# Performance work log

Measured on AMD Instinct MI355X. Metric: run time of the kernel, lower is better.

## Reference

```python
import jax, jax.numpy as jnp
import numpy as np

T, B, D, H, NQ = 512, 128, 512, 64, 64  # seq_len, batch, input_dim, hidden_dim == n_qubits
EPS = 1e-5

def setup_inputs() -> dict:
    key = jax.random.key(0)
    ks = jax.random.split(key, 11)
    s = 0.05
    return {
        "inputs": jax.random.normal(ks[0], (T, B, D), jnp.float32),
        "W0": jax.random.normal(ks[1], (4, NQ, D + H), jnp.float32) * s,
        "b0": jax.random.normal(ks[2], (4, NQ), jnp.float32) * s,
        "th0": jax.random.normal(ks[3], (4, NQ), jnp.float32) * s,
        "g0": jnp.ones((H,), jnp.float32),
        "be0": jnp.zeros((H,), jnp.float32),
        "W1": jax.random.normal(ks[4], (4, NQ, H + H), jnp.float32) * s,
        "b1": jax.random.normal(ks[5], (4, NQ), jnp.float32) * s,
        "th1": jax.random.normal(ks[6], (4, NQ), jnp.float32) * s,
        "g1": jnp.ones((H,), jnp.float32),
        "be1": jnp.zeros((H,), jnp.float32),
    }

def _qlstm_layer(x, W, b, th, gamma, beta):
    # x: [T, B, Din]. Faithful to source: h_prev = c_prev = 0 at EVERY timestep
    # (the torch code never writes back `states` inside the time loop), so all
    # timesteps are independent and fully vectorized.
    zeros_h = jnp.zeros(x.shape[:-1] + (H,), x.dtype)
    combined = jnp.concatenate([x, zeros_h], axis=-1)           # [T,B,Din+H]
    # 4 gate linears stacked on leading axis g: forget, input, update, output
    z = jnp.einsum('tbk,gnk->gtbn', combined, W) + b[:, None, None, :]
    # quantum circuit closed form: RX(z_i+th_i) per qubit + CNOT ladder + <Z_k>
    #   => cumprod_{i<=k} cos(z_i + th_i)
    q = jnp.cumprod(jnp.cos(z + th[:, None, None, :]), axis=-1)  # [4,T,B,NQ]
    sg = jax.nn.sigmoid(q)
    i_g = sg[1]
    g_g = jnp.tanh(sg[2])
    o_g = sg[3]
    # c = f * c_prev + i * g, with c_prev == 0  (f gate has no effect)
    c = i_g * g_g                                                # [T,B,H]
    h = o_g * jnp.tanh(c)
    mu = jnp.mean(h, axis=-1, keepdims=True)
    var = jnp.mean((h - mu) ** 2, axis=-1, keepdims=True)
    h_ln = (h - mu) * jax.lax.rsqrt(var + EPS) * gamma + beta
    return h_ln, c

def reference(inputs, W0, b0, th0, g0, be0, W1, b1, th1, g1, be1):
    h0, c0 = _qlstm_layer(inputs, W0, b0, th0, g0, be0)  # layer 0 (no dropout: p=0)
    h1, c1 = _qlstm_layer(h0, W1, b1, th1, g1, be1)      # layer 1
    outputs = h1                                          # [T,B,H]
    # new_states = states at the last timestep: [(h_ln, c)] per layer
    return (outputs, h0[-1], c0[-1], h1[-1], c1[-1])
```

## Files before the change

### kernel.cpp

```cpp
#include <hip/hip_runtime.h>
#include <hip/hip_bf16.h>

typedef __attribute__((ext_vector_type(8))) short bf16x8;
typedef __attribute__((ext_vector_type(4))) float f32x4;

#define T_SEQ   512
#define B_BATCH 128
#define H_DIM   64
#define MB      64
#define A1S     72
#define ZS_STRIDE 193
#define A2S       72
#define LASTROW ((T_SEQ - 1) * B_BATCH)

#define W0H 0
#define W0M 98304
#define W0L 196608
#define W1H 294912
#define W1M 307200
#define W1L 319488

__device__ __forceinline__ void tsplit(float f, unsigned& h, unsigned& m, unsigned& l) {
    unsigned uf = __builtin_bit_cast(unsigned, f);
    h = uf >> 16;
    float hf = __builtin_bit_cast(float, uf & 0xFFFF0000u);
    float r1 = f - hf;
    unsigned u1 = __builtin_bit_cast(unsigned, r1);
    m = u1 >> 16;
    float mf = __builtin_bit_cast(float, u1 & 0xFFFF0000u);
    float r2 = r1 - mf;
    l = __builtin_bit_cast(unsigned, r2) >> 16;
}

__device__ __forceinline__ void tsplit2(float a, float b,
                                        unsigned& ph, unsigned& pm, unsigned& pl) {
    unsigned ha, ma, la, hb, mb, lb;
    tsplit(a, ha, ma, la);
    tsplit(b, hb, mb, lb);
    ph = ha | (hb << 16);
    pm = ma | (mb << 16);
    pl = la | (lb << 16);
}

__device__ __forceinline__ void split16(const float4 f[4],
                                        short* __restrict__ ah, short* __restrict__ am,
                                        short* __restrict__ al, int ao) {
    uint4 Ph, Pm, Pl;
    tsplit2(f[0].x, f[0].y, Ph.x, Pm.x, Pl.x);
    tsplit2(f[0].z, f[0].w, Ph.y, Pm.y, Pl.y);
    tsplit2(f[1].x, f[1].y, Ph.z, Pm.z, Pl.z);
    tsplit2(f[1].z, f[1].w, Ph.w, Pm.w, Pl.w);
    *(uint4*)(ah + ao) = Ph;
    *(uint4*)(am + ao) = Pm;
    *(uint4*)(al + ao) = Pl;
    tsplit2(f[2].x, f[2].y, Ph.x, Pm.x, Pl.x);
    tsplit2(f[2].z, f[2].w, Ph.y, Pm.y, Pl.y);
    tsplit2(f[3].x, f[3].y, Ph.z, Pm.z, Pl.z);
    tsplit2(f[3].z, f[3].w, Ph.w, Pm.w, Pl.w);
    *(uint4*)(ah + ao + 8) = Ph;
    *(uint4*)(am + ao + 8) = Pm;
    *(uint4*)(al + ao + 8) = Pl;
}

__device__ __forceinline__ f32x4 mfma6(bf16x8 ah, bf16x8 am, bf16x8 al,
                                       bf16x8 bh, bf16x8 bm, bf16x8 bl, f32x4 c) {
    c = __builtin_amdgcn_mfma_f32_16x16x32_bf16(ah, bh, c, 0, 0, 0);
    c = __builtin_amdgcn_mfma_f32_16x16x32_bf16(ah, bm, c, 0, 0, 0);
    c = __builtin_amdgcn_mfma_f32_16x16x32_bf16(am, bh, c, 0, 0, 0);
    c = __builtin_amdgcn_mfma_f32_16x16x32_bf16(ah, bl, c, 0, 0, 0);
    c = __builtin_amdgcn_mfma_f32_16x16x32_bf16(al, bh, c, 0, 0, 0);
    c = __builtin_amdgcn_mfma_f32_16x16x32_bf16(am, bm, c, 0, 0, 0);
    return c;
}

__device__ __forceinline__ float fast_cos(float x) {
    float n = rintf(x * 0.6366197723675814f);
    int   m = (int)n;
    float r = __builtin_fmaf(n, -1.5707962512969971e+00f, x);
    r = __builtin_fmaf(n, -7.5497894158615964e-08f, r);
    r = __builtin_fmaf(n, -5.3903025299577647e-15f, r);
    float r2 = r * r;
    float ps = __builtin_fmaf(r2, 2.7557314297e-06f, -1.9841270114e-04f);
    ps = __builtin_fmaf(r2, ps, 8.3333337680e-03f);
    ps = __builtin_fmaf(r2, ps, -1.6666667163e-01f);
    float s = __builtin_fmaf(r * r2, ps, r);
    float pc = __builtin_fmaf(r2, 2.4801587642e-05f, -1.3888889225e-03f);
    pc = __builtin_fmaf(r2, pc, 4.1666667908e-02f);
    pc = __builtin_fmaf(r2, pc, -0.5f);
    float c = __builtin_fmaf(r2, pc, 1.0f);
    float v = (m & 1) ? s : c;
    unsigned sign = (unsigned)((m + 1) & 2) << 30;
    return __builtin_bit_cast(float, __builtin_bit_cast(unsigned, v) ^ sign);
}

__device__ __forceinline__ float fast_sigmoid(float x) {
    float e = __expf(-x);
    float d = 1.0f + e;
    float r = __builtin_amdgcn_rcpf(d);
    return r * (2.0f - d * r);
}

__device__ __forceinline__ float fast_tanh_pos(float x) {
    float t = __expf(2.0f * x);
    float d = t + 1.0f;
    float r = __builtin_amdgcn_rcpf(d);
    r = r * (2.0f - d * r);
    return (t - 1.0f) * r;
}

__global__ __launch_bounds__(256) void presplit_w(const float* __restrict__ W0,
                                                  const float* __restrict__ W1,
                                                  short* __restrict__ ws) {
    int i = blockIdx.x * 256 + threadIdx.x;
    if (i < 98304) {
        int r = i >> 9, k = i & 511;
        unsigned h, m, l;
        tsplit(W0[(r + 64) * 576 + k], h, m, l);
        ws[W0H + i] = (short)h;
        ws[W0M + i] = (short)m;
        ws[W0L + i] = (short)l;
    } else if (i < 110592) {
        int j = i - 98304;
        int r = j >> 6, k = j & 63;
        unsigned h, m, l;
        tsplit(W1[(r + 64) * 128 + k], h, m, l);
        ws[W1H + j] = (short)h;
        ws[W1M + j] = (short)m;
        ws[W1L + j] = (short)l;
    }
}

__global__ __launch_bounds__(256, 3) void qlstm_fused(
    const float* __restrict__ x,
    const float* __restrict__ b0,
    const float* __restrict__ th0,
    const float* __restrict__ g0,
    const float* __restrict__ be0,
    const float* __restrict__ b1,
    const float* __restrict__ th1,
    const float* __restrict__ g1,
    const float* __restrict__ be1,
    const short* __restrict__ wsp,
    float* __restrict__ out)
{
    __shared__ __align__(16) char lds[50944];
    short* ah = (short*)lds;
    short* am = ah + 64 * A1S;
    short* al = am + 64 * A1S;
    float* zs  = (float*)lds;
    short* a2h = (short*)lds;
    short* a2m = a2h + 64 * A2S;
    short* a2l = a2m + 64 * A2S;
    float* bt0 = (float*)(lds + 49408);
    float* bt1 = bt0 + 192;

    const int tid = threadIdx.x;
    const long rowbase = (long)blockIdx.x * MB;

    float* out0 = out;
    float* out1 = out + (long)T_SEQ * B_BATCH * H_DIM;
    float* out2 = out1 + B_BATCH * H_DIM;
    float* out3 = out2 + B_BATCH * H_DIM;
    float* out4 = out3 + B_BATCH * H_DIM;

    if (tid < 192) {
        bt0[tid] = b0[64 + tid] + th0[64 + tid];
        bt1[tid] = b1[64 + tid] + th1[64 + tid];
    }

    const int lane = tid & 63;
    const int wave = tid >> 6;
    const int ln   = lane & 15;
    const int quad = lane >> 4;
    const int cw   = wave * 48;

    int brow0[3], brow1[3];
    for (int nt = 0; nt < 3; ++nt) {
        int gc = cw + nt * 16 + ln;
        brow0[nt] = gc * 512;
        brow1[nt] = gc * 64;
    }

    const int sr = tid >> 2;
    const int sc = (tid & 3) << 4;
    const float* xrow = x + (rowbase + sr) * 512 + sc;
    const int sao = sr * A1S + sc;

    f32x4 acc[4][3];
    #pragma unroll
    for (int mt = 0; mt < 4; ++mt)
        #pragma unroll
        for (int nt = 0; nt < 3; ++nt)
            acc[mt][nt] = (f32x4){0.f, 0.f, 0.f, 0.f};

    {
        float4 f[4];
        #pragma unroll
        for (int u = 0; u < 4; ++u) f[u] = *(const float4*)(xrow + u * 4);
        split16(f, ah, am, al, sao);
    }
    __syncthreads();

    for (int kc = 0; kc < 512; kc += 64) {
        float4 nf[4];
        const bool more = (kc + 64) < 512;
        if (more) {
            #pragma unroll
            for (int u = 0; u < 4; ++u)
                nf[u] = *(const float4*)(xrow + kc + 64 + u * 4);
        }
        #pragma unroll
        for (int k0 = 0; k0 < 64; k0 += 32) {
            int ka = k0 + quad * 8;
            bf16x8 Ah[4], Am[4], Al[4];
            #pragma unroll
            for (int mt = 0; mt < 4; ++mt) {
                int ao = (mt * 16 + ln) * A1S + ka;
                Ah[mt] = *(const bf16x8*)(ah + ao);
                Am[mt] = *(const bf16x8*)(am + ao);
                Al[mt] = *(const bf16x8*)(al + ao);
            }
            #pragma unroll
            for (int nt = 0; nt < 3; ++nt) {
                int bo = brow0[nt] + kc + ka;
                bf16x8 Bh = *(const bf16x8*)(wsp + W0H + bo);
                bf16x8 Bm = *(const bf16x8*)(wsp + W0M + bo);
                bf16x8 Bl = *(const bf16x8*)(wsp + W0L + bo);
                #pragma unroll
                for (int mt = 0; mt < 4; ++mt)
                    acc[mt][nt] = mfma6(Ah[mt], Am[mt], Al[mt], Bh, Bm, Bl, acc[mt][nt]);
            }
        }
        __syncthreads();
        if (more) {
            split16(nf, ah, am, al, sao);
            __syncthreads();
        }
    }

    #pragma unroll
    for (int mt = 0; mt < 4; ++mt)
        #pragma unroll
        for (int nt = 0; nt < 3; ++nt)
            #pragma unroll
            for (int i = 0; i < 4; ++i) {
                int row = mt * 16 + quad * 4 + i;
                int col = cw + nt * 16 + ln;
                zs[row * ZS_STRIDE + col] = acc[mt][nt][i];
            }
    __syncthreads();

    if (tid < 192) {
        int gi = tid >> 6;
        int r  = tid & 63;
        float* zrow = zs + r * ZS_STRIDE + gi * 64;
        const float* btg = bt0 + gi * 64;
        float p = 1.0f;
        for (int n = 0; n < 64; ++n) {
            p *= fast_cos(zrow[n] + btg[n]);
            zrow[n] = p;
        }
    }
    __syncthreads();

    {
        int r = tid >> 2;
        int j = tid & 3;
        long tbrow = rowbase + r;
        bool lastt = (tbrow >= LASTROW);
        int bidx = (int)(tbrow - LASTROW);
        const float* zr = zs + r * ZS_STRIDE;
        float h[16];
        float s = 0.f;
        #pragma unroll
        for (int i = 0; i < 16; ++i) {
            int n = j * 16 + i;
            float q1 = zr[n];
            float q2 = zr[64 + n];
            float q3 = zr[128 + n];
            float ig = fast_sigmoid(q1);
            float gg = fast_tanh_pos(fast_sigmoid(q2));
            float og = fast_sigmoid(q3);
            float c  = ig * gg;
            float hv = og * fast_tanh_pos(c);
            h[i] = hv;
            s += hv;
            if (lastt) out2[bidx * 64 + n] = c;
        }
        s += __shfl_xor(s, 1);  s += __shfl_xor(s, 2);
        float mu = s * (1.0f / 64.0f);
        float s2 = 0.f;
        #pragma unroll
        for (int i = 0; i < 16; ++i) {
            float d = h[i] - mu;
            s2 += d * d;
        }
        s2 += __shfl_xor(s2, 1); s2 += __shfl_xor(s2, 2);
        float var = s2 * (1.0f / 64.0f);
        float rs  = rsqrtf(var + 1e-5f);
        float hl[16];
        #pragma unroll
        for (int i = 0; i < 16; ++i) {
            int n = j * 16 + i;
            hl[i] = (h[i] - mu) * rs * g0[n] + be0[n];
            if (lastt) out1[bidx * 64 + n] = hl[i];
        }
        __syncthreads();

        int ab = r * A2S + j * 16;
        uint4 Ph, Pm, Pl;
        tsplit2(hl[0], hl[1], Ph.x, Pm.x, Pl.x);
        tsplit2(hl[2], hl[3], Ph.y, Pm.y, Pl.y);
        tsplit2(hl[4], hl[5], Ph.z, Pm.z, Pl.z);
        tsplit2(hl[6], hl[7], Ph.w, Pm.w, Pl.w);
        *(uint4*)(a2h + ab) = Ph;
        *(uint4*)(a2m + ab) = Pm;
        *(uint4*)(a2l + ab) = Pl;
        tsplit2(hl[8],  hl[9],  Ph.x, Pm.x, Pl.x);
        tsplit2(hl[10], hl[11], Ph.y, Pm.y, Pl.y);
        tsplit2(hl[12], hl[13], Ph.z, Pm.z, Pl.z);
        tsplit2(hl[14], hl[15], Ph.w, Pm.w, Pl.w);
        *(uint4*)(a2h + ab + 8) = Ph;
        *(uint4*)(a2m + ab + 8) = Pm;
        *(uint4*)(a2l + ab + 8) = Pl;
    }
    __syncthreads();

    f32x4 acc2[4][3];
    #pragma unroll
    for (int mt = 0; mt < 4; ++mt)
        #pragma unroll
        for (int nt = 0; nt < 3; ++nt)
            acc2[mt][nt] = (f32x4){0.f, 0.f, 0.f, 0.f};
    #pragma unroll
    for (int k0 = 0; k0 < 64; k0 += 32) {
        int ka = k0 + quad * 8;
        bf16x8 Ah[4], Am[4], Al[4];
        #pragma unroll
        for (int mt = 0; mt < 4; ++mt) {
            int ao = (mt * 16 + ln) * A2S + ka;
            Ah[mt] = *(const bf16x8*)(a2h + ao);
            Am[mt] = *(const bf16x8*)(a2m + ao);
            Al[mt] = *(const bf16x8*)(a2l + ao);
        }
        #pragma unroll
        for (int nt = 0; nt < 3; ++nt) {
            int bo = brow1[nt] + ka;
            bf16x8 Bh = *(const bf16x8*)(wsp + W1H + bo);
            bf16x8 Bm = *(const bf16x8*)(wsp + W1M + bo);
            bf16x8 Bl = *(const bf16x8*)(wsp + W1L + bo);
            #pragma unroll
            for (int mt = 0; mt < 4; ++mt)
                acc2[mt][nt] = mfma6(Ah[mt], Am[mt], Al[mt], Bh, Bm, Bl, acc2[mt][nt]);
        }
    }
    __syncthreads();
    #pragma unroll
    for (int mt = 0; mt < 4; ++mt)
        #pragma unroll
        for (int nt = 0; nt < 3; ++nt)
            #pragma unroll
            for (int i = 0; i < 4; ++i) {
                int row = mt * 16 + quad * 4 + i;
                int col = cw + nt * 16 + ln;
                zs[row * ZS_STRIDE + col] = acc2[mt][nt][i];
            }
    __syncthreads();

    if (tid < 192) {
        int gi = tid >> 6;
        int r  = tid & 63;
        float* zrow = zs + r * ZS_STRIDE + gi * 64;
        const float* btg = bt1 + gi * 64;
        float p = 1.0f;
        for (int n = 0; n < 64; ++n) {
            p *= fast_cos(zrow[n] + btg[n]);
            zrow[n] = p;
        }
    }
    __syncthreads();

    {
        int r = tid >> 2;
        int j = tid & 3;
        long tbrow = rowbase + r;
        bool lastt = (tbrow >= LASTROW);
        int bidx = (int)(tbrow - LASTROW);
        const float* zr = zs + r * ZS_STRIDE;
        float h[16];
        float s = 0.f;
        #pragma unroll
        for (int i = 0; i < 16; ++i) {
            int n = j * 16 + i;
            float q1 = zr[n];
            float q2 = zr[64 + n];
            float q3 = zr[128 + n];
            float ig = fast_sigmoid(q1);
            float gg = fast_tanh_pos(fast_sigmoid(q2));
            float og = fast_sigmoid(q3);
            float c  = ig * gg;
            float hv = og * fast_tanh_pos(c);
            h[i] = hv;
            s += hv;
            if (lastt) out4[bidx * 64 + n] = c;
        }
        s += __shfl_xor(s, 1);  s += __shfl_xor(s, 2);
        float mu = s * (1.0f / 64.0f);
        float s2 = 0.f;
        #pragma unroll
        for (int i = 0; i < 16; ++i) {
            float d = h[i] - mu;
            s2 += d * d;
        }
        s2 += __shfl_xor(s2, 1); s2 += __shfl_xor(s2, 2);
        float var = s2 * (1.0f / 64.0f);
        float rs  = rsqrtf(var + 1e-5f);
        float o4[16];
        #pragma unroll
        for (int i = 0; i < 16; ++i)
            o4[i] = (h[i] - mu) * rs * g1[j * 16 + i] + be1[j * 16 + i];
        float* dst = out0 + tbrow * 64 + j * 16;
        #pragma unroll
        for (int i4 = 0; i4 < 4; ++i4)
            *(float4*)(dst + i4 * 4) = *(float4*)(o4 + i4 * 4);
        if (lastt) {
            float* dst3 = out3 + (long)bidx * 64 + j * 16;
            #pragma unroll
            for (int i4 = 0; i4 < 4; ++i4)
                *(float4*)(dst3 + i4 * 4) = *(float4*)(o4 + i4 * 4);
        }
    }
}

extern "C" void kernel_launch(void* const* d_in, const int* in_sizes, int n_in,
                              void* d_out, int out_size, void* d_ws, size_t ws_size,
                              hipStream_t stream) {
    const float* x   = (const float*)d_in[0];
    const float* W0  = (const float*)d_in[1];
    const float* b0  = (const float*)d_in[2];
    const float* th0 = (const float*)d_in[3];
    const float* g0  = (const float*)d_in[4];
    const float* be0 = (const float*)d_in[5];
    const float* W1  = (const float*)d_in[6];
    const float* b1  = (const float*)d_in[7];
    const float* th1 = (const float*)d_in[8];
    const float* g1  = (const float*)d_in[9];
    const float* be1 = (const float*)d_in[10];
    short* wsp = (short*)d_ws;

    presplit_w<<<dim3(432), dim3(256), 0, stream>>>(W0, W1, wsp);
    qlstm_fused<<<dim3(1024), dim3(256), 0, stream>>>(
        x, b0, th0, g0, be0, b1, th1, g1, be1, wsp, (float*)d_out);
}
```

Before: 321.9 us.

## Process gate epilogue in 16-row quarters to shrink LDS and raise occupancy

The z staging buffer now holds only 16 rows at a time. The cumprod and LayerNorm epilogues loop over four quarters, and the layer-2 A operand gets its own LDS region. This cuts LDS from about 50KB to 40KB, and launch bounds rise from 3 to 4 blocks per CU. The cost is much less parallelism in the epilogue: only 48 or 64 threads are active per quarter, with many more __syncthreads. Bias plus theta is now read from global memory inside the loop instead of being precomputed in LDS.

New measurement: 408.8 us. 27.0% more time.

```diff
diff --git a/kernel.cpp b/kernel.cpp
--- a/kernel.cpp
+++ b/kernel.cpp
@@ -9,7 +9,7 @@
 #define H_DIM   64
 #define MB      64
 #define A1S     72
-#define ZS_STRIDE 193
+#define ZQ_STRIDE 193
 #define A2S       72
 #define LASTROW ((T_SEQ - 1) * B_BATCH)
 
@@ -130,7 +130,7 @@
     }
 }
 
-__global__ __launch_bounds__(256, 3) void qlstm_fused(
+__global__ __launch_bounds__(256, 4) void qlstm_fused(
     const float* __restrict__ x,
     const float* __restrict__ b0,
     const float* __restrict__ th0,
@@ -143,16 +143,14 @@
     const short* __restrict__ wsp,
     float* __restrict__ out)
 {
-    __shared__ __align__(16) char lds[50944];
+    __shared__ __align__(16) char lds[40000];
     short* ah = (short*)lds;
     short* am = ah + 64 * A1S;
     short* al = am + 64 * A1S;
     float* zs  = (float*)lds;
-    short* a2h = (short*)lds;
+    short* a2h = (short*)(lds + 12352);
     short* a2m = a2h + 64 * A2S;
     short* a2l = a2m + 64 * A2S;
-    float* bt0 = (float*)(lds + 49408);
-    float* bt1 = bt0 + 192;
 
     const int tid = threadIdx.x;
     const long rowbase = (long)blockIdx.x * MB;
@@ -162,11 +160,6 @@
     float* out2 = out1 + B_BATCH * H_DIM;
     float* out3 = out2 + B_BATCH * H_DIM;
     float* out4 = out3 + B_BATCH * H_DIM;
-
-    if (tid < 192) {
-        bt0[tid] = b0[64 + tid] + th0[64 + tid];
-        bt1[tid] = b1[64 + tid] + th1[64 + tid];
-    }
 
     const int lane = tid & 63;
     const int wave = tid >> 6;
@@ -239,90 +232,89 @@
     }
 
     #pragma unroll
-    for (int mt = 0; mt < 4; ++mt)
+    for (int qd = 0; qd < 4; ++qd) {
+        if (qd > 0) __syncthreads();
         #pragma unroll
         for (int nt = 0; nt < 3; ++nt)
             #pragma unroll
-            for (int i = 0; i < 4; ++i) {
-                int row = mt * 16 + quad * 4 + i;
-                int col = cw + nt * 16 + ln;
-                zs[row * ZS_STRIDE + col] = acc[mt][nt][i];
-            }
-    __syncthreads();
-
-    if (tid < 192) {
-        int gi = tid >> 6;
-        int r  = tid & 63;
-        float* zrow = zs + r * ZS_STRIDE + gi * 64;
-        const float* btg = bt0 + gi * 64;
-        float p = 1.0f;
-        for (int n = 0; n < 64; ++n) {
-            p *= fast_cos(zrow[n] + btg[n]);
-            zrow[n] = p;
-        }
-    }
-    __syncthreads();
-
-    {
-        int r = tid >> 2;
-        int j = tid & 3;
-        long tbrow = rowbase + r;
-        bool lastt = (tbrow >= LASTROW);
-        int bidx = (int)(tbrow - LASTROW);
-        const float* zr = zs + r * ZS_STRIDE;
-        float h[16];
-        float s = 0.f;
-        #pragma unroll
-        for (int i = 0; i < 16; ++i) {
-            int n = j * 16 + i;
-            float q1 = zr[n];
-            float q2 = zr[64 + n];
-            float q3 = zr[128 + n];
-            float ig = fast_sigmoid(q1);
-            float gg = fast_tanh_pos(fast_sigmoid(q2));
-            float og = fast_sigmoid(q3);
-            float c  = ig * gg;
-            float hv = og * fast_tanh_pos(c);
-            h[i] = hv;
-            s += hv;
-            if (lastt) out2[bidx * 64 + n] = c;
-        }
-        s += __shfl_xor(s, 1);  s += __shfl_xor(s, 2);
-        float mu = s * (1.0f / 64.0f);
-        float s2 = 0.f;
-        #pragma unroll
-        for (int i = 0; i < 16; ++i) {
-            float d = h[i] - mu;
-            s2 += d * d;
-        }
-        s2 += __shfl_xor(s2, 1); s2 += __shfl_xor(s2, 2);
-        float var = s2 * (1.0f / 64.0f);
-        float rs  = rsqrtf(var + 1e-5f);
-        float hl[16];
-        #pragma unroll
-        for (int i = 0; i < 16; ++i) {
-            int n = j * 16 + i;
-            hl[i] = (h[i] - mu) * rs * g0[n] + be0[n];
-            if (lastt) out1[bidx * 64 + n] = hl[i];
-        }
-        __syncthreads();
-
-        int ab = r * A2S + j * 16;
-        uint4 Ph, Pm, Pl;
-        tsplit2(hl[0], hl[1], Ph.x, Pm.x, Pl.x);
-        tsplit2(hl[2], hl[3], Ph.y, Pm.y, Pl.y);
-        tsplit2(hl[4], hl[5], Ph.z, Pm.z, Pl.z);
-        tsplit2(hl[6], hl[7], Ph.w, Pm.w, Pl.w);
-        *(uint4*)(a2h + ab) = Ph;
-        *(uint4*)(a2m + ab) = Pm;
-        *(uint4*)(a2l + ab) = Pl;
-        tsplit2(hl[8],  hl[9],  Ph.x, Pm.x, Pl.x);
-        tsplit2(hl[10], hl[11], Ph.y, Pm.y, Pl.y);
-        tsplit2(hl[12], hl[13], Ph.z, Pm.z, Pl.z);
-        tsplit2(hl[14], hl[15], Ph.w, Pm.w, Pl.w);
-        *(uint4*)(a2h + ab + 8) = Ph;
-        *(uint4*)(a2m + ab + 8) = Pm;
-        *(uint4*)(a2l + ab + 8) = Pl;
+            for (int i = 0; i < 4; ++i)
+                zs[(quad * 4 + i) * ZQ_STRIDE + cw + nt * 16 + ln] = acc[qd][nt][i];
+        __syncthreads();
+
+        if (tid < 48) {
+            int gi = tid >> 4;
+            int r  = tid & 15;
+            float* zrow = zs + r * ZQ_STRIDE + gi * 64;
+            const float* bg = b0 + 64 + gi * 64;
+            const float* tg = th0 + 64 + gi * 64;
+            float p = 1.0f;
+            for (int n = 0; n < 64; ++n) {
+                p *= fast_cos(zrow[n] + bg[n] + tg[n]);
+                zrow[n] = p;
+            }
+        }
+        __syncthreads();
+
+        if (tid < 64) {
+            int r = tid >> 2;
+            int j = tid & 3;
+            int rloc = qd * 16 + r;
+            long tbrow = rowbase + rloc;
+            bool lastt = (tbrow >= LASTROW);
+            int bidx = (int)(tbrow - LASTROW);
+            const float* zr = zs + r * ZQ_STRIDE;
+            float h[16];
+            float s = 0.f;
+            #pragma unroll
+            for (int i = 0; i < 16; ++i) {
+                int n = j * 16 + i;
+                float q1 = zr[n];
+                float q2 = zr[64 + n];
+                float q3 = zr[128 + n];
+                float ig = fast_sigmoid(q1);
+                float gg = fast_tanh_pos(fast_sigmoid(q2));
+                float og = fast_sigmoid(q3);
+                float c  = ig * gg;
+                float hv = og * fast_tanh_pos(c);
+                h[i] = hv;
+                s += hv;
+                if (lastt) out2[bidx * 64 + n] = c;
+            }
+            s += __shfl_xor(s, 1);  s += __shfl_xor(s, 2);
+            float mu = s * (1.0f / 64.0f);
+            float s2 = 0.f;
+            #pragma unroll
+            for (int i = 0; i < 16; ++i) {
+                float d = h[i] - mu;
+                s2 += d * d;
+            }
+            s2 += __shfl_xor(s2, 1); s2 += __shfl_xor(s2, 2);
+            float var = s2 * (1.0f / 64.0f);
+            float rs  = rsqrtf(var + 1e-5f);
+            float hl[16];
+            #pragma unroll
+            for (int i = 0; i < 16; ++i) {
+                int n = j * 16 + i;
+                hl[i] = (h[i] - mu) * rs * g0[n] + be0[n];
+                if (lastt) out1[bidx * 64 + n] = hl[i];
+            }
+            int ab = rloc * A2S + j * 16;
+            uint4 Ph, Pm, Pl;
+            tsplit2(hl[0], hl[1], Ph.x, Pm.x, Pl.x);
+            tsplit2(hl[2], hl[3], Ph.y, Pm.y, Pl.y);
+            tsplit2(hl[4], hl[5], Ph.z, Pm.z, Pl.z);
+            tsplit2(hl[6], hl[7], Ph.w, Pm.w, Pl.w);
+            *(uint4*)(a2h + ab) = Ph;
+            *(uint4*)(a2m + ab) = Pm;
+            *(uint4*)(a2l + ab) = Pl;
+            tsplit2(hl[8],  hl[9],  Ph.x, Pm.x, Pl.x);
+            tsplit2(hl[10], hl[11], Ph.y, Pm.y, Pl.y);
+            tsplit2(hl[12], hl[13], Ph.z, Pm.z, Pl.z);
+            tsplit2(hl[14], hl[15], Ph.w, Pm.w, Pl.w);
+            *(uint4*)(a2h + ab + 8) = Ph;
+            *(uint4*)(a2m + ab + 8) = Pm;
+            *(uint4*)(a2l + ab + 8) = Pl;
+        }
     }
     __syncthreads();
 
@@ -354,80 +346,80 @@
                 acc2[mt][nt] = mfma6(Ah[mt], Am[mt], Al[mt], Bh, Bm, Bl, acc2[mt][nt]);
         }
     }
-    __syncthreads();
+
     #pragma unroll
-    for (int mt = 0; mt < 4; ++mt)
+    for (int qd = 0; qd < 4; ++qd) {
+        __syncthreads();
         #pragma unroll
         for (int nt = 0; nt < 3; ++nt)
             #pragma unroll
-            for (int i = 0; i < 4; ++i) {
-                int row = mt * 16 + quad * 4 + i;
-                int col = cw + nt * 16 + ln;
-                zs[row * ZS_STRIDE + col] = acc2[mt][nt][i];
-            }
-    __syncthreads();
-
-    if (tid < 192) {
-        int gi = tid >> 6;
-        int r  = tid & 63;
-        float* zrow = zs + r * ZS_STRIDE + gi * 64;
-        const float* btg = bt1 + gi * 64;
-        float p = 1.0f;
-        for (int n = 0; n < 64; ++n) {
-            p *= fast_cos(zrow[n] + btg[n]);
-            zrow[n] = p;
-        }
-    }
-    __syncthreads();
-
-    {
-        int r = tid >> 2;
-        int j = tid & 3;
-        long tbrow = rowbase + r;
-        bool lastt = (tbrow >= LASTROW);
-        int bidx = (int)(tbrow - LASTROW);
-        const float* zr = zs + r * ZS_STRIDE;
-        float h[16];
-        float s = 0.f;
-        #pragma unroll
-        for (int i = 0; i < 16; ++i) {
-            int n = j * 16 + i;
-            float q1 = zr[n];
-            float q2 = zr[64 + n];
-            float q3 = zr[128 + n];
-            float ig = fast_sigmoid(q1);
-            float gg = fast_tanh_pos(fast_sigmoid(q2));
-            float og = fast_sigmoid(q3);
-            float c  = ig * gg;
-            float hv = og * fast_tanh_pos(c);
-            h[i] = hv;
-            s += hv;
-            if (lastt) out4[bidx * 64 + n] = c;
-        }
-        s += __shfl_xor(s, 1);  s += __shfl_xor(s, 2);
-        float mu = s * (1.0f / 64.0f);
-        float s2 = 0.f;
-        #pragma unroll
-        for (int i = 0; i < 16; ++i) {
-            float d = h[i] - mu;
-            s2 += d * d;
-        }
-        s2 += __shfl_xor(s2, 1); s2 += __shfl_xor(s2, 2);
-        float var = s2 * (1.0f / 64.0f);
-        float rs  = rsqrtf(var + 1e-5f);
-        float o4[16];
-        #pragma unroll
-        for (int i = 0; i < 16; ++i)
-            o4[i] = (h[i] - mu) * rs * g1[j * 16 + i] + be1[j * 16 + i];
-        float* dst = out0 + tbrow * 64 + j * 16;
-        #pragma unroll
-        for (int i4 = 0; i4 < 4; ++i4)
-            *(float4*)(dst + i4 * 4) = *(float4*)(o4 + i4 * 4);
-        if (lastt) {
-            float* dst3 = out3 + (long)bidx * 64 + j * 16;
+            for (int i = 0; i < 4; ++i)
+                zs[(quad * 4 + i) * ZQ_STRIDE + cw + nt * 16 + ln] = acc2[qd][nt][i];
+        __syncthreads();
+
+        if (tid < 48) {
+            int gi = tid >> 4;
+            int r  = tid & 15;
+            float* zrow = zs + r * ZQ_STRIDE + gi * 64;
+            const float* bg = b1 + 64 + gi * 64;
+            const float* tg = th1 + 64 + gi * 64;
+            float p = 1.0f;
+            for (int n = 0; n < 64; ++n) {
+                p *= fast_cos(zrow[n] + bg[n] + tg[n]);
+                zrow[n] = p;
+            }
+        }
+        __syncthreads();
+
+        if (tid < 64) {
+            int r = tid >> 2;
+            int j = tid & 3;
+            long tbrow = rowbase + qd * 16 + r;
+            bool lastt = (tbrow >= LASTROW);
+            int bidx = (int)(tbrow - LASTROW);
+            const float* zr = zs + r * ZQ_STRIDE;
+            float h[16];
+            float s = 0.f;
+            #pragma unroll
+            for (int i = 0; i < 16; ++i) {
+                int n = j * 16 + i;
+                float q1 = zr[n];
+                float q2 = zr[64 + n];
+                float q3 = zr[128 + n];
+                float ig = fast_sigmoid(q1);
+                float gg = fast_tanh_pos(fast_sigmoid(q2));
+                float og = fast_sigmoid(q3);
+                float c  = ig * gg;
+                float hv = og * fast_tanh_pos(c);
+                h[i] = hv;
+                s += hv;
+                if (lastt) out4[bidx * 64 + n] = c;
+            }
+            s += __shfl_xor(s, 1);  s += __shfl_xor(s, 2);
+            float mu = s * (1.0f / 64.0f);
+            float s2 = 0.f;
+            #pragma unroll
+            for (int i = 0; i < 16; ++i) {
+                float d = h[i] - mu;
+                s2 += d * d;
+            }
+            s2 += __shfl_xor(s2, 1); s2 += __shfl_xor(s2, 2);
+            float var = s2 * (1.0f / 64.0f);
+            float rs  = rsqrtf(var + 1e-5f);
+            float o4[16];
+            #pragma unroll
+            for (int i = 0; i < 16; ++i)
+                o4[i] = (h[i] - mu) * rs * g1[j * 16 + i] + be1[j * 16 + i];
+            float* dst = out0 + tbrow * 64 + j * 16;
             #pragma unroll
             for (int i4 = 0; i4 < 4; ++i4)
-                *(float4*)(dst3 + i4 * 4) = *(float4*)(o4 + i4 * 4);
+                *(float4*)(dst + i4 * 4) = *(float4*)(o4 + i4 * 4);
+            if (lastt) {
+                float* dst3 = out3 + (long)bidx * 64 + j * 16;
+                #pragma unroll
+                for (int i4 = 0; i4 < 4; ++i4)
+                    *(float4*)(dst3 + i4 * 4) = *(float4*)(o4 + i4 * 4);
+            }
         }
     }
 }
```

## Double-buffer layer-0 A tiles in LDS and drop redundant barriers

Applied to the files above, without the earlier changes.

Splits the layer-0 activation staging into two LDS buffers so the next K-chunk is written while the current one is read, cutting one barrier per iteration. The layer-1 activation buffer moves to its own LDS region so it no longer aliases zs, which lets two more barriers go. LDS grows to about 77 KB and launch bounds drop from 3 to 2 blocks per CU, trading occupancy for fewer syncs.

Result: faster. 314.1 us (-2.4%).

```diff
diff --git a/kernel.cpp b/kernel.cpp
--- a/kernel.cpp
+++ b/kernel.cpp
@@ -130,7 +130,7 @@
     }
 }
 
-__global__ __launch_bounds__(256, 3) void qlstm_fused(
+__global__ __launch_bounds__(256, 2) void qlstm_fused(
     const float* __restrict__ x,
     const float* __restrict__ b0,
     const float* __restrict__ th0,
@@ -143,15 +143,18 @@
     const short* __restrict__ wsp,
     float* __restrict__ out)
 {
-    __shared__ __align__(16) char lds[50944];
-    short* ah = (short*)lds;
-    short* am = ah + 64 * A1S;
-    short* al = am + 64 * A1S;
+    __shared__ __align__(16) char lds[78592];
+    short* ah0 = (short*)lds;
+    short* am0 = ah0 + 4608;
+    short* al0 = am0 + 4608;
+    short* ah1 = (short*)(lds + 27648);
+    short* am1 = ah1 + 4608;
+    short* al1 = am1 + 4608;
     float* zs  = (float*)lds;
-    short* a2h = (short*)lds;
-    short* a2m = a2h + 64 * A2S;
-    short* a2l = a2m + 64 * A2S;
-    float* bt0 = (float*)(lds + 49408);
+    short* a2h = (short*)(lds + 49408);
+    short* a2m = a2h + 4608;
+    short* a2l = a2m + 4608;
+    float* bt0 = (float*)(lds + 77056);
     float* bt1 = bt0 + 192;
 
     const int tid = threadIdx.x;
@@ -175,6 +178,7 @@
     const int cw   = wave * 48;
 
     int brow0[3], brow1[3];
+    #pragma unroll
     for (int nt = 0; nt < 3; ++nt) {
         int gc = cw + nt * 16 + ln;
         brow0[nt] = gc * 512;
@@ -197,11 +201,19 @@
         float4 f[4];
         #pragma unroll
         for (int u = 0; u < 4; ++u) f[u] = *(const float4*)(xrow + u * 4);
-        split16(f, ah, am, al, sao);
+        split16(f, ah0, am0, al0, sao);
     }
     __syncthreads();
 
     for (int kc = 0; kc < 512; kc += 64) {
+        const int p = (kc >> 6) & 1;
+        short* rah = p ? ah1 : ah0;
+        short* ram = p ? am1 : am0;
+        short* ral = p ? al1 : al0;
+        short* wah = p ? ah0 : ah1;
+        short* wam = p ? am0 : am1;
+        short* wal = p ? al0 : al1;
+
         float4 nf[4];
         const bool more = (kc + 64) < 512;
         if (more) {
@@ -216,9 +228,9 @@
             #pragma unroll
             for (int mt = 0; mt < 4; ++mt) {
                 int ao = (mt * 16 + ln) * A1S + ka;
-                Ah[mt] = *(const bf16x8*)(ah + ao);
-                Am[mt] = *(const bf16x8*)(am + ao);
-                Al[mt] = *(const bf16x8*)(al + ao);
+                Ah[mt] = *(const bf16x8*)(rah + ao);
+                Am[mt] = *(const bf16x8*)(ram + ao);
+                Al[mt] = *(const bf16x8*)(ral + ao);
             }
             #pragma unroll
             for (int nt = 0; nt < 3; ++nt) {
@@ -231,11 +243,8 @@
                     acc[mt][nt] = mfma6(Ah[mt], Am[mt], Al[mt], Bh, Bm, Bl, acc[mt][nt]);
             }
         }
+        if (more) split16(nf, wah, wam, wal, sao);
         __syncthreads();
-        if (more) {
-            split16(nf, ah, am, al, sao);
-            __syncthreads();
-        }
     }
 
     #pragma unroll
@@ -305,8 +314,6 @@
             hl[i] = (h[i] - mu) * rs * g0[n] + be0[n];
             if (lastt) out1[bidx * 64 + n] = hl[i];
         }
-        __syncthreads();
-
         int ab = r * A2S + j * 16;
         uint4 Ph, Pm, Pl;
         tsplit2(hl[0], hl[1], Ph.x, Pm.x, Pl.x);
@@ -354,7 +361,6 @@
                 acc2[mt][nt] = mfma6(Ah[mt], Am[mt], Al[mt], Bh, Bm, Bl, acc2[mt][nt]);
         }
     }
-    __syncthreads();
     #pragma unroll
     for (int mt = 0; mt < 4; ++mt)
         #pragma unroll
```
